# Optimization experiments

Measured on AMD Instinct MI355X. Metric: run time of the kernel, lower is better.

## Reference

```python
import jax, jax.numpy as jnp
import numpy as np

N_NODES = 50000
N_EDGES = 800000
IN_FEATS = 128
HIDDEN = 64
EDGE_FEATS = 3


def setup_inputs() -> dict:
    key = jax.random.key(0)
    ks = jax.random.split(key, 8)
    s = lambda d: 1.0 / np.sqrt(d)
    return {
        "x": jax.random.normal(ks[0], (N_NODES, IN_FEATS), jnp.float32),
        "efeat": jax.random.normal(ks[1], (N_EDGES, EDGE_FEATS), jnp.float32),
        "src": jax.random.randint(ks[2], (N_EDGES,), 0, N_NODES, jnp.int32),
        "dst": jax.random.randint(ks[3], (N_EDGES,), 0, N_NODES, jnp.int32),
        "W1": jax.random.normal(ks[4], (IN_FEATS, HIDDEN), jnp.float32) * s(IN_FEATS),
        "b1": jnp.zeros((HIDDEN,), jnp.float32),
        "W2": jax.random.normal(ks[5], (HIDDEN, HIDDEN), jnp.float32) * s(HIDDEN),
        "b2": jnp.zeros((HIDDEN,), jnp.float32),
        "We": jax.random.normal(ks[6], (2 * HIDDEN + EDGE_FEATS, 1), jnp.float32) * s(2 * HIDDEN + EDGE_FEATS),
        "be": jnp.zeros((1,), jnp.float32),
    }


def reference(x, efeat, src, dst, W1, b1, W2, b2, We, be):
    n = x.shape[0]
    ones = jnp.ones(src.shape[0], x.dtype)
    # DGL GraphConv norm='both': scale src feats by out-deg^-1/2, aggregate, scale by in-deg^-1/2
    deg_out = jnp.clip(jax.ops.segment_sum(ones, src, num_segments=n), 1.0)
    deg_in = jnp.clip(jax.ops.segment_sum(ones, dst, num_segments=n), 1.0)
    c_src = deg_out ** -0.5  # [N]
    c_dst = deg_in ** -0.5   # [N]

    def graph_conv(h, W, b):
        hn = h * c_src[:, None]                             # pre-scale
        agg = jax.ops.segment_sum(hn[src], dst, num_segments=n)
        return (agg * c_dst[:, None]) @ W + b

    h = jax.nn.relu(graph_conv(x, W1, b1))
    h = graph_conv(h, W2, b2)

    # edge_func: sigmoid(Linear(cat[src_h, dst_h, efeat])) -- split We to avoid concat
    H = h.shape[1]
    Ws, Wd, Wf = We[:H], We[H:2 * H], We[2 * H:]
    logits = h[src] @ Ws + h[dst] @ Wd + efeat @ Wf + be   # [E, 1]
    return jax.nn.sigmoid(logits[:, 0])                    # [E]
```

## Files before the change

### kernel.cpp

```cpp
#include <hip/hip_runtime.h>
#include <math.h>
#include <stdint.h>

#define N_NODES 50000
#define N_EDGES 800000
#define IN_FEATS 128
#define HIDDEN 64

#define CSPLIT 32
#define CHUNK (N_EDGES / CSPLIT)
#define NQUART (N_NODES / 4)
#define NQWORDS (NQUART / 2)

#define NB_HIST 256
#define NB_E4 782
#define NB_GEMM 782

typedef __attribute__((ext_vector_type(8))) short bf16x8;
typedef __attribute__((ext_vector_type(4))) float f32x4;

__device__ __forceinline__ unsigned short f2bf(float f) {
    unsigned u = __float_as_uint(f);
    u = (u + 0x7FFF + ((u >> 16) & 1)) >> 16;
    return (unsigned short)u;
}

#define ACC8F(A, r, cs)                                        \
    A[0] = fmaf(cs, __uint_as_float((r).x << 16), A[0]);       \
    A[1] = fmaf(cs, __uint_as_float((r).x & 0xffff0000u), A[1]); \
    A[2] = fmaf(cs, __uint_as_float((r).y << 16), A[2]);       \
    A[3] = fmaf(cs, __uint_as_float((r).y & 0xffff0000u), A[3]); \
    A[4] = fmaf(cs, __uint_as_float((r).z << 16), A[4]);       \
    A[5] = fmaf(cs, __uint_as_float((r).z & 0xffff0000u), A[5]); \
    A[6] = fmaf(cs, __uint_as_float((r).w << 16), A[6]);       \
    A[7] = fmaf(cs, __uint_as_float((r).w & 0xffff0000u), A[7]);

__global__ __launch_bounds__(256) void hist_gemm_kernel(const int* __restrict__ src,
                                                        const int* __restrict__ dst,
                                                        unsigned short* __restrict__ epos,
                                                        unsigned* __restrict__ pin,
                                                        unsigned* __restrict__ pout,
                                                        const float* __restrict__ x,
                                                        const float* __restrict__ W,
                                                        unsigned short* __restrict__ yb) {
    __shared__ union {
        unsigned cnt[NQWORDS];
        bf16x8 bfrag[16][64];
    } u;
    if (blockIdx.x < NB_HIST) {
        int b = blockIdx.x;
        int c = b >> 3;
        int kind = (b >> 2) & 1;
        int quar = b & 3;
        int lo = quar * NQUART;
        for (int i = threadIdx.x; i < NQWORDS; i += 256) u.cnt[i] = 0;
        __syncthreads();
        if (kind == 0) {
            const int4* d4 = reinterpret_cast<const int4*>(dst + c * CHUNK);
            for (int i = threadIdx.x; i < CHUNK / 4; i += 256) {
                int4 d = d4[i];
                int e = c * CHUNK + i * 4;
                unsigned q, old;
                q = (unsigned)(d.x - lo);
                if (q < NQUART) { old = atomicAdd(&u.cnt[q >> 1], 1u << ((q & 1) * 16));
                                  epos[e + 0] = (unsigned short)(old >> ((q & 1) * 16)); }
                q = (unsigned)(d.y - lo);
                if (q < NQUART) { old = atomicAdd(&u.cnt[q >> 1], 1u << ((q & 1) * 16));
                                  epos[e + 1] = (unsigned short)(old >> ((q & 1) * 16)); }
                q = (unsigned)(d.z - lo);
                if (q < NQUART) { old = atomicAdd(&u.cnt[q >> 1], 1u << ((q & 1) * 16));
                                  epos[e + 2] = (unsigned short)(old >> ((q & 1) * 16)); }
                q = (unsigned)(d.w - lo);
                if (q < NQUART) { old = atomicAdd(&u.cnt[q >> 1], 1u << ((q & 1) * 16));
                                  epos[e + 3] = (unsigned short)(old >> ((q & 1) * 16)); }
            }
        } else {
            const int4* s4 = reinterpret_cast<const int4*>(src + c * CHUNK);
            for (int i = threadIdx.x; i < CHUNK / 4; i += 256) {
                int4 s = s4[i];
                unsigned q;
                q = (unsigned)(s.x - lo); if (q < NQUART) atomicAdd(&u.cnt[q >> 1], 1u << ((q & 1) * 16));
                q = (unsigned)(s.y - lo); if (q < NQUART) atomicAdd(&u.cnt[q >> 1], 1u << ((q & 1) * 16));
                q = (unsigned)(s.z - lo); if (q < NQUART) atomicAdd(&u.cnt[q >> 1], 1u << ((q & 1) * 16));
                q = (unsigned)(s.w - lo); if (q < NQUART) atomicAdd(&u.cnt[q >> 1], 1u << ((q & 1) * 16));
            }
        }
        __syncthreads();
        unsigned* outp = (kind ? pout : pin) + c * (N_NODES / 2) + quar * NQWORDS;
        for (int i = threadIdx.x; i < NQWORDS; i += 256) outp[i] = u.cnt[i];
        return;
    }
    int gb = blockIdx.x - NB_HIST;
    for (int idx = threadIdx.x; idx < 16 * 64; idx += 256) {
        int f = idx >> 6, l = idx & 63;
        int nt = f >> 2, kt = f & 3;
        int col = nt * 16 + (l & 15);
        int k0 = kt * 32 + (l >> 4) * 8;
        bf16x8 bv;
#pragma unroll
        for (int j = 0; j < 8; ++j) bv[j] = (short)f2bf(W[(k0 + j) * HIDDEN + col]);
        u.bfrag[f][l] = bv;
    }
    __syncthreads();
    int wid = threadIdx.x >> 6, l = threadIdx.x & 63;
    bf16x8 Breg[16];
#pragma unroll
    for (int f = 0; f < 16; ++f) Breg[f] = u.bfrag[f][l];

    int row0 = gb * 64 + wid * 16;
    int arow = row0 + (l & 15);
    int asafe = min(arow, N_NODES - 1);
    const float* xr = x + (size_t)asafe * IN_FEATS + (l >> 4) * 8;
    f32x4 acc0 = {0.f, 0.f, 0.f, 0.f};
    f32x4 acc1 = {0.f, 0.f, 0.f, 0.f};
    f32x4 acc2 = {0.f, 0.f, 0.f, 0.f};
    f32x4 acc3 = {0.f, 0.f, 0.f, 0.f};
#pragma unroll
    for (int kt = 0; kt < 4; ++kt) {
        float4 a0 = *reinterpret_cast<const float4*>(xr + kt * 32);
        float4 a1 = *reinterpret_cast<const float4*>(xr + kt * 32 + 4);
        bf16x8 av;
        av[0] = (short)f2bf(a0.x); av[1] = (short)f2bf(a0.y);
        av[2] = (short)f2bf(a0.z); av[3] = (short)f2bf(a0.w);
        av[4] = (short)f2bf(a1.x); av[5] = (short)f2bf(a1.y);
        av[6] = (short)f2bf(a1.z); av[7] = (short)f2bf(a1.w);
        acc0 = __builtin_amdgcn_mfma_f32_16x16x32_bf16(av, Breg[0 * 4 + kt], acc0, 0, 0, 0);
        acc1 = __builtin_amdgcn_mfma_f32_16x16x32_bf16(av, Breg[1 * 4 + kt], acc1, 0, 0, 0);
        acc2 = __builtin_amdgcn_mfma_f32_16x16x32_bf16(av, Breg[2 * 4 + kt], acc2, 0, 0, 0);
        acc3 = __builtin_amdgcn_mfma_f32_16x16x32_bf16(av, Breg[3 * 4 + kt], acc3, 0, 0, 0);
    }
#pragma unroll
    for (int i = 0; i < 4; ++i) {
        int row = row0 + (l >> 4) * 4 + i;
        if (row < N_NODES) {
            unsigned short* yr = yb + (size_t)row * HIDDEN + (l & 15);
            yr[0]  = f2bf(acc0[i]);
            yr[16] = f2bf(acc1[i]);
            yr[32] = f2bf(acc2[i]);
            yr[48] = f2bf(acc3[i]);
        }
    }
}

__global__ __launch_bounds__(256) void prep_kernel(const unsigned* __restrict__ pin,
                                                   const unsigned* __restrict__ pout,
                                                   float* __restrict__ cs,
                                                   float* __restrict__ cd,
                                                   int* __restrict__ offs,
                                                   int* __restrict__ bsum,
                                                   const float* __restrict__ W2,
                                                   const float* __restrict__ We,
                                                   const float* __restrict__ b2,
                                                   float* __restrict__ w2s,
                                                   float* __restrict__ w2d,
                                                   float* __restrict__ w2c) {
    int b = blockIdx.x;
    int t = threadIdx.x;
    if (b == 49) {
        if (t < 64) {
            float s = 0.f, d = 0.f;
            for (int j = 0; j < HIDDEN; ++j) {
                float w = W2[t * HIDDEN + j];
                s = fmaf(w, We[j], s);
                d = fmaf(w, We[HIDDEN + j], d);
            }
            w2s[t] = s;
            w2d[t] = d;
        } else if (t == 64) {
            float s = 0.f, d = 0.f;
            for (int j = 0; j < HIDDEN; ++j) {
                s = fmaf(We[j], b2[j], s);
                d = fmaf(We[HIDDEN + j], b2[j], d);
            }
            w2c[0] = s;
            w2c[1] = d;
        }
        return;
    }
    __shared__ int sums[256];
    int v0 = b * 1024 + t * 4;
    bool ok = v0 < N_NODES;
    unsigned si0 = 0, si1 = 0, si2 = 0, si3 = 0;
    unsigned so0 = 0, so1 = 0, so2 = 0, so3 = 0;
    if (ok) {
        int w0 = v0 >> 1;
#pragma unroll
        for (int c = 0; c < CSPLIT; ++c) {
            uint2 a = *reinterpret_cast<const uint2*>(pin + (size_t)c * (N_NODES / 2) + w0);
            uint2 o = *reinterpret_cast<const uint2*>(pout + (size_t)c * (N_NODES / 2) + w0);
            si0 += a.x & 0xffffu; si1 += a.x >> 16;
            si2 += a.y & 0xffffu; si3 += a.y >> 16;
            so0 += o.x & 0xffffu; so1 += o.x >> 16;
            so2 += o.y & 0xffffu; so3 += o.y >> 16;
        }
        *reinterpret_cast<float4*>(cs + v0) =
            make_float4(rsqrtf(fmaxf((float)so0, 1.f)), rsqrtf(fmaxf((float)so1, 1.f)),
                        rsqrtf(fmaxf((float)so2, 1.f)), rsqrtf(fmaxf((float)so3, 1.f)));
        *reinterpret_cast<float4*>(cd + v0) =
            make_float4(rsqrtf(fmaxf((float)si0, 1.f)), rsqrtf(fmaxf((float)si1, 1.f)),
                        rsqrtf(fmaxf((float)si2, 1.f)), rsqrtf(fmaxf((float)si3, 1.f)));
    }
    int d0 = (int)si0, d1 = (int)si1, d2 = (int)si2, d3 = (int)si3;
    sums[t] = d0 + d1 + d2 + d3;
    __syncthreads();
    for (int o = 1; o < 256; o <<= 1) {
        int v = (t >= o) ? sums[t - o] : 0;
        __syncthreads();
        sums[t] += v;
        __syncthreads();
    }
    int excl = (t == 0) ? 0 : sums[t - 1];
    if (ok) {
        *reinterpret_cast<int4*>(offs + v0) =
            make_int4(excl, excl + d0, excl + d0 + d1, excl + d0 + d1 + d2);
    }
    if (t == 255) bsum[b] = sums[255];
}

__global__ __launch_bounds__(256) void scan3_base_kernel(int* __restrict__ offs,
                                                         const int* __restrict__ bsum,
                                                         const unsigned* __restrict__ pin,
                                                         unsigned short* __restrict__ baser) {
    __shared__ int sbase[64];
    int t = threadIdx.x;
    if (t < 64) {
        int val = (t < 49) ? bsum[t] : 0;
        int s = val;
#pragma unroll
        for (int o = 1; o < 64; o <<= 1) {
            int u = __shfl_up(s, o, 64);
            if (t >= o) s += u;
        }
        sbase[t] = s - val;
    }
    __syncthreads();
    int v = blockIdx.x * 256 + t;
    if (v >= N_NODES) return;
    int off = offs[v] + sbase[v >> 10];
    offs[v] = off;
    int rel = 0;
    int sh = (v & 1) * 16;
#pragma unroll
    for (int c = 0; c < CSPLIT; ++c) {
        baser[(size_t)c * N_NODES + v] = (unsigned short)rel;
        rel += (int)((pin[(size_t)c * (N_NODES / 2) + (v >> 1)] >> sh) & 0xffffu);
    }
    if (v == 0) offs[N_NODES] = N_EDGES;
}

__global__ __launch_bounds__(256) void fill_kernel(const int* __restrict__ src,
                                                   const int* __restrict__ dst,
                                                   const unsigned short* __restrict__ epos,
                                                   const int* __restrict__ offs,
                                                   const unsigned short* __restrict__ baser,
                                                   int* __restrict__ csr_src) {
    int t = blockIdx.x * 256 + threadIdx.x;
    int e0 = t * 4;
    if (e0 >= N_EDGES) return;
    int c = e0 / CHUNK;
    const unsigned short* brc = baser + (size_t)c * N_NODES;
    int4 s = *reinterpret_cast<const int4*>(src + e0);
    int4 d = *reinterpret_cast<const int4*>(dst + e0);
    ushort4 ep = *reinterpret_cast<const ushort4*>(epos + e0);
    csr_src[offs[d.x] + brc[d.x] + ep.x] = s.x;
    csr_src[offs[d.y] + brc[d.y] + ep.y] = s.y;
    csr_src[offs[d.z] + brc[d.z] + ep.z] = s.z;
    csr_src[offs[d.w] + brc[d.w] + ep.w] = s.w;
}

__global__ __launch_bounds__(256) void gather_t_kernel(const unsigned short* __restrict__ y,
                                                       const int* __restrict__ offs,
                                                       const int* __restrict__ csr_src,
                                                       const float* __restrict__ c_src,
                                                       const float* __restrict__ c_dst,
                                                       const float* __restrict__ b1,
                                                       const float* __restrict__ w2s,
                                                       const float* __restrict__ w2d,
                                                       float2* __restrict__ t) {
    int wid = threadIdx.x >> 6, l = threadIdx.x & 63;
    int slot = l >> 3, q8 = l & 7;
    int v0 = blockIdx.x * 8 + wid * 2;
    int v1 = v0 + 1;
    int beg0 = offs[v0], end0 = offs[v0 + 1], end1 = offs[v0 + 2];
    int k0 = beg0, k1 = end0;
    float acc0[8] = {0.f, 0.f, 0.f, 0.f, 0.f, 0.f, 0.f, 0.f};
    float acc1[8] = {0.f, 0.f, 0.f, 0.f, 0.f, 0.f, 0.f, 0.f};
    while (k0 + 8 <= end0 && k1 + 8 <= end1) {
        int sA = csr_src[k0 + slot];
        int sB = csr_src[k1 + slot];
        float csA = c_src[sA];
        float csB = c_src[sB];
        uint4 rA = *reinterpret_cast<const uint4*>(y + (size_t)sA * HIDDEN + q8 * 8);
        uint4 rB = *reinterpret_cast<const uint4*>(y + (size_t)sB * HIDDEN + q8 * 8);
        ACC8F(acc0, rA, csA);
        ACC8F(acc1, rB, csB);
        k0 += 8;
        k1 += 8;
    }
    while (k0 + 8 <= end0) {
        int s = csr_src[k0 + slot];
        float cs = c_src[s];
        uint4 r = *reinterpret_cast<const uint4*>(y + (size_t)s * HIDDEN + q8 * 8);
        ACC8F(acc0, r, cs);
        k0 += 8;
    }
    while (k1 + 8 <= end1) {
        int s = csr_src[k1 + slot];
        float cs = c_src[s];
        uint4 r = *reinterpret_cast<const uint4*>(y + (size_t)s * HIDDEN + q8 * 8);
        ACC8F(acc1, r, cs);
        k1 += 8;
    }
    if (slot < end0 - k0) {
        int s = csr_src[k0 + slot];
        float cs = c_src[s];
        uint4 r = *reinterpret_cast<const uint4*>(y + (size_t)s * HIDDEN + q8 * 8);
        ACC8F(acc0, r, cs);
    }
    if (slot < end1 - k1) {
        int s = csr_src[k1 + slot];
        float cs = c_src[s];
        uint4 r = *reinterpret_cast<const uint4*>(y + (size_t)s * HIDDEN + q8 * 8);
        ACC8F(acc1, r, cs);
    }
#pragma unroll
    for (int i = 0; i < 8; ++i) {
        acc0[i] += __shfl_xor(acc0[i], 8, 64);
        acc0[i] += __shfl_xor(acc0[i], 16, 64);
        acc0[i] += __shfl_xor(acc0[i], 32, 64);
        acc1[i] += __shfl_xor(acc1[i], 8, 64);
        acc1[i] += __shfl_xor(acc1[i], 16, 64);
        acc1[i] += __shfl_xor(acc1[i], 32, 64);
    }
    float4 ba = *reinterpret_cast<const float4*>(b1 + q8 * 8);
    float4 bb = *reinterpret_cast<const float4*>(b1 + q8 * 8 + 4);
    float4 wsa = *reinterpret_cast<const float4*>(w2s + q8 * 8);
    float4 wsb = *reinterpret_cast<const float4*>(w2s + q8 * 8 + 4);
    float4 wda = *reinterpret_cast<const float4*>(w2d + q8 * 8);
    float4 wdb = *reinterpret_cast<const float4*>(w2d + q8 * 8 + 4);
    float c0 = c_dst[v0], c1 = c_dst[v1];
    float h0, h1, h2, h3, h4, h5, h6, h7;
    h0 = fmaxf(fmaf(c0, acc0[0], ba.x), 0.f);
    h1 = fmaxf(fmaf(c0, acc0[1], ba.y), 0.f);
    h2 = fmaxf(fmaf(c0, acc0[2], ba.z), 0.f);
    h3 = fmaxf(fmaf(c0, acc0[3], ba.w), 0.f);
    h4 = fmaxf(fmaf(c0, acc0[4], bb.x), 0.f);
    h5 = fmaxf(fmaf(c0, acc0[5], bb.y), 0.f);
    h6 = fmaxf(fmaf(c0, acc0[6], bb.z), 0.f);
    h7 = fmaxf(fmaf(c0, acc0[7], bb.w), 0.f);
    float ps0 = h0 * wsa.x + h1 * wsa.y + h2 * wsa.z + h3 * wsa.w
              + h4 * wsb.x + h5 * wsb.y + h6 * wsb.z + h7 * wsb.w;
    float pd0 = h0 * wda.x + h1 * wda.y + h2 * wda.z + h3 * wda.w
              + h4 * wdb.x + h5 * wdb.y + h6 * wdb.z + h7 * wdb.w;
    h0 = fmaxf(fmaf(c1, acc1[0], ba.x), 0.f);
    h1 = fmaxf(fmaf(c1, acc1[1], ba.y), 0.f);
    h2 = fmaxf(fmaf(c1, acc1[2], ba.z), 0.f);
    h3 = fmaxf(fmaf(c1, acc1[3], ba.w), 0.f);
    h4 = fmaxf(fmaf(c1, acc1[4], bb.x), 0.f);
    h5 = fmaxf(fmaf(c1, acc1[5], bb.y), 0.f);
    h6 = fmaxf(fmaf(c1, acc1[6], bb.z), 0.f);
    h7 = fmaxf(fmaf(c1, acc1[7], bb.w), 0.f);
    float ps1 = h0 * wsa.x + h1 * wsa.y + h2 * wsa.z + h3 * wsa.w
              + h4 * wsb.x + h5 * wsb.y + h6 * wsb.z + h7 * wsb.w;
    float pd1 = h0 * wda.x + h1 * wda.y + h2 * wda.z + h3 * wda.w
              + h4 * wdb.x + h5 * wdb.y + h6 * wdb.z + h7 * wdb.w;
#pragma unroll
    for (int o = 1; o <= 4; o <<= 1) {
        ps0 += __shfl_xor(ps0, o, 64);
        pd0 += __shfl_xor(pd0, o, 64);
        ps1 += __shfl_xor(ps1, o, 64);
        pd1 += __shfl_xor(pd1, o, 64);
    }
    if (l == 0) {
        float cs0 = c_src[v0], cs1 = c_src[v1];
        *reinterpret_cast<float4*>(t + v0) =
            make_float4(cs0 * ps0, cs0 * pd0, cs1 * ps1, cs1 * pd1);
    }
}

__global__ __launch_bounds__(256) void gather2_kernel(const float2* __restrict__ t,
                                                      const int* __restrict__ offs,
                                                      const int* __restrict__ csr_src,
                                                      const float* __restrict__ c_dst,
                                                      const float* __restrict__ w2c,
                                                      float* __restrict__ a_s,
                                                      float* __restrict__ a_d) {
    int wid = threadIdx.x >> 6, l = threadIdx.x & 63;
    int sub = l >> 4, q = l & 15;
    int v = blockIdx.x * 16 + wid * 4 + sub;
    int beg = offs[v], end = offs[v + 1];
    float ps = 0.f, pd = 0.f;
    for (int k = beg + q; k < end; k += 16) {
        float2 tv = t[csr_src[k]];
        ps += tv.x;
        pd += tv.y;
    }
#pragma unroll
    for (int o = 1; o <= 8; o <<= 1) {
        ps += __shfl_xor(ps, o, 64);
        pd += __shfl_xor(pd, o, 64);
    }
    if (q == 0) {
        float c = c_dst[v];
        a_s[v] = fmaf(c, ps, w2c[0]);
        a_d[v] = fmaf(c, pd, w2c[1]);
    }
}

__global__ __launch_bounds__(256) void edge_out_kernel(const int* __restrict__ src,
                                                       const int* __restrict__ dst,
                                                       const float* __restrict__ efeat,
                                                       const float* __restrict__ We,
                                                       const float* __restrict__ be,
                                                       const float* __restrict__ a_s,
                                                       const float* __restrict__ a_d,
                                                       float* __restrict__ out) {
    int t = blockIdx.x * 256 + threadIdx.x;
    int e0 = t * 8;
    if (e0 >= N_EDGES) return;
    float w0 = We[2 * HIDDEN + 0], w1 = We[2 * HIDDEN + 1], w2 = We[2 * HIDDEN + 2];
    float b = be[0];
    int4 sA = *reinterpret_cast<const int4*>(src + e0);
    int4 sB = *reinterpret_cast<const int4*>(src + e0 + 4);
    int4 dA = *reinterpret_cast<const int4*>(dst + e0);
    int4 dB = *reinterpret_cast<const int4*>(dst + e0 + 4);
    const float4* f = reinterpret_cast<const float4*>(efeat + (long)e0 * 3);
    float4 f0 = f[0], f1 = f[1], f2 = f[2], f3 = f[3], f4 = f[4], f5 = f[5];
    float as0 = a_s[sA.x], as1 = a_s[sA.y], as2 = a_s[sA.z], as3 = a_s[sA.w];
    float as4 = a_s[sB.x], as5 = a_s[sB.y], as6 = a_s[sB.z], as7 = a_s[sB.w];
    float ad0 = a_d[dA.x], ad1 = a_d[dA.y], ad2 = a_d[dA.z], ad3 = a_d[dA.w];
    float ad4 = a_d[dB.x], ad5 = a_d[dB.y], ad6 = a_d[dB.z], ad7 = a_d[dB.w];
    float4 oA, oB;
    float z;
    z = as0 + ad0 + f0.x * w0 + f0.y * w1 + f0.z * w2 + b;
    oA.x = 1.0f / (1.0f + __expf(-z));
    z = as1 + ad1 + f0.w * w0 + f1.x * w1 + f1.y * w2 + b;
    oA.y = 1.0f / (1.0f + __expf(-z));
    z = as2 + ad2 + f1.z * w0 + f1.w * w1 + f2.x * w2 + b;
    oA.z = 1.0f / (1.0f + __expf(-z));
    z = as3 + ad3 + f2.y * w0 + f2.z * w1 + f2.w * w2 + b;
    oA.w = 1.0f / (1.0f + __expf(-z));
    z = as4 + ad4 + f3.x * w0 + f3.y * w1 + f3.z * w2 + b;
    oB.x = 1.0f / (1.0f + __expf(-z));
    z = as5 + ad5 + f3.w * w0 + f4.x * w1 + f4.y * w2 + b;
    oB.y = 1.0f / (1.0f + __expf(-z));
    z = as6 + ad6 + f4.z * w0 + f4.w * w1 + f5.x * w2 + b;
    oB.z = 1.0f / (1.0f + __expf(-z));
    z = as7 + ad7 + f5.y * w0 + f5.z * w1 + f5.w * w2 + b;
    oB.w = 1.0f / (1.0f + __expf(-z));
    *reinterpret_cast<float4*>(out + e0) = oA;
    *reinterpret_cast<float4*>(out + e0 + 4) = oB;
}

extern "C" void kernel_launch(void* const* d_in, const int* in_sizes, int n_in,
                              void* d_out, int out_size, void* d_ws, size_t ws_size,
                              hipStream_t stream) {
    const float* x     = (const float*)d_in[0];
    const float* efeat = (const float*)d_in[1];
    const int*   src   = (const int*)d_in[2];
    const int*   dst   = (const int*)d_in[3];
    const float* W1    = (const float*)d_in[4];
    const float* b1    = (const float*)d_in[5];
    const float* W2    = (const float*)d_in[6];
    const float* b2    = (const float*)d_in[7];
    const float* We    = (const float*)d_in[8];
    const float* be    = (const float*)d_in[9];
    float* out = (float*)d_out;

    char* p = (char*)d_ws;
    auto alloc = [&](size_t bytes) {
        char* r = p;
        p += (bytes + 255) & ~(size_t)255;
        return r;
    };
    float* c_src   = (float*)alloc((size_t)N_NODES * 4);
    float* c_dst   = (float*)alloc((size_t)N_NODES * 4);
    float* a_s     = (float*)alloc((size_t)N_NODES * 4);
    float* a_d     = (float*)alloc((size_t)N_NODES * 4);
    int*   offs    = (int*)alloc((size_t)(N_NODES + 1) * 4);
    int*   bsum    = (int*)alloc(64 * 4);
    float* w2s     = (float*)alloc(HIDDEN * 4);
    float* w2d     = (float*)alloc(HIDDEN * 4);
    float* w2c     = (float*)alloc(2 * 4);
    unsigned*       pin   = (unsigned*)alloc((size_t)CSPLIT * (N_NODES / 2) * 4);
    unsigned*       pout  = (unsigned*)alloc((size_t)CSPLIT * (N_NODES / 2) * 4);
    unsigned short* epos  = (unsigned short*)alloc((size_t)N_EDGES * 2);
    unsigned short* baser = (unsigned short*)alloc((size_t)CSPLIT * N_NODES * 2);
    int*            csr_src = (int*)alloc((size_t)N_EDGES * 4);
    unsigned short* yb    = (unsigned short*)alloc((size_t)N_NODES * HIDDEN * 2);
    float2*         t     = (float2*)alloc((size_t)N_NODES * 8);

    const int NB_V = (N_NODES + 255) / 256;

    hist_gemm_kernel<<<NB_HIST + NB_GEMM, 256, 0, stream>>>(src, dst, epos, pin, pout,
                                                            x, W1, yb);
    prep_kernel<<<50, 256, 0, stream>>>(pin, pout, c_src, c_dst, offs, bsum,
                                        W2, We, b2, w2s, w2d, w2c);
    scan3_base_kernel<<<NB_V, 256, 0, stream>>>(offs, bsum, pin, baser);
    fill_kernel<<<NB_E4, 256, 0, stream>>>(src, dst, epos, offs, baser, csr_src);
    gather_t_kernel<<<N_NODES / 8, 256, 0, stream>>>(yb, offs, csr_src, c_src, c_dst,
                                                     b1, w2s, w2d, t);
    gather2_kernel<<<N_NODES / 16, 256, 0, stream>>>(t, offs, csr_src, c_dst, w2c, a_s, a_d);
    edge_out_kernel<<<(N_EDGES / 8 + 255) / 256, 256, 0, stream>>>(src, dst, efeat, We, be,
                                                                   a_s, a_d, out);
}
```

Measured before the change: 93.53 us.

## Split bf16 hidden features into two 32-wide planes for gather kernel

The GEMM output is stored as two separate planes of 32 features each, and the first gather kernel runs twice as many blocks, each handling one plane with 16 edge slots of 4 lanes. Partial t values are written per plane and summed in gather2, which now reads a float4 per source node. The aim is a smaller per-pass working set for random row gathers, so each plane fits better in cache, and more edge-level parallelism per wave. In exchange, csr_src and offsets are read twice, there is an extra shuffle stage, and t doubles in size.

```diff
diff --git a/kernel.cpp b/kernel.cpp
--- a/kernel.cpp
+++ b/kernel.cpp
@@ -15,6 +15,8 @@
 #define NB_HIST 256
 #define NB_E4 782
 #define NB_GEMM 782
+#define NBG 6250
+#define PLANE_ELEMS ((size_t)N_NODES * 32)
 
 typedef __attribute__((ext_vector_type(8))) short bf16x8;
 typedef __attribute__((ext_vector_type(4))) float f32x4;
@@ -133,11 +135,12 @@
     for (int i = 0; i < 4; ++i) {
         int row = row0 + (l >> 4) * 4 + i;
         if (row < N_NODES) {
-            unsigned short* yr = yb + (size_t)row * HIDDEN + (l & 15);
-            yr[0]  = f2bf(acc0[i]);
-            yr[16] = f2bf(acc1[i]);
-            yr[32] = f2bf(acc2[i]);
-            yr[48] = f2bf(acc3[i]);
+            unsigned short* y0 = yb + (size_t)row * 32 + (l & 15);
+            unsigned short* y1 = y0 + PLANE_ELEMS;
+            y0[0]  = f2bf(acc0[i]);
+            y0[16] = f2bf(acc1[i]);
+            y1[0]  = f2bf(acc2[i]);
+            y1[16] = f2bf(acc3[i]);
         }
     }
 }
@@ -277,77 +280,83 @@
                                                        const float* __restrict__ w2s,
                                                        const float* __restrict__ w2d,
                                                        float2* __restrict__ t) {
+    int plane = (blockIdx.x >= NBG) ? 1 : 0;
+    int bb = blockIdx.x - plane * NBG;
+    const unsigned short* yp = y + (size_t)plane * PLANE_ELEMS;
     int wid = threadIdx.x >> 6, l = threadIdx.x & 63;
-    int slot = l >> 3, q8 = l & 7;
-    int v0 = blockIdx.x * 8 + wid * 2;
+    int slot = l >> 2, q4 = l & 3;
+    int v0 = bb * 8 + wid * 2;
     int v1 = v0 + 1;
     int beg0 = offs[v0], end0 = offs[v0 + 1], end1 = offs[v0 + 2];
     int k0 = beg0, k1 = end0;
     float acc0[8] = {0.f, 0.f, 0.f, 0.f, 0.f, 0.f, 0.f, 0.f};
     float acc1[8] = {0.f, 0.f, 0.f, 0.f, 0.f, 0.f, 0.f, 0.f};
-    while (k0 + 8 <= end0 && k1 + 8 <= end1) {
+    while (k0 + 16 <= end0 && k1 + 16 <= end1) {
         int sA = csr_src[k0 + slot];
         int sB = csr_src[k1 + slot];
         float csA = c_src[sA];
         float csB = c_src[sB];
-        uint4 rA = *reinterpret_cast<const uint4*>(y + (size_t)sA * HIDDEN + q8 * 8);
-        uint4 rB = *reinterpret_cast<const uint4*>(y + (size_t)sB * HIDDEN + q8 * 8);
+        uint4 rA = *reinterpret_cast<const uint4*>(yp + (size_t)sA * 32 + q4 * 8);
+        uint4 rB = *reinterpret_cast<const uint4*>(yp + (size_t)sB * 32 + q4 * 8);
         ACC8F(acc0, rA, csA);
         ACC8F(acc1, rB, csB);
-        k0 += 8;
-        k1 += 8;
-    }
-    while (k0 + 8 <= end0) {
+        k0 += 16;
+        k1 += 16;
+    }
+    while (k0 + 16 <= end0) {
         int s = csr_src[k0 + slot];
         float cs = c_src[s];
-        uint4 r = *reinterpret_cast<const uint4*>(y + (size_t)s * HIDDEN + q8 * 8);
+        uint4 r = *reinterpret_cast<const uint4*>(yp + (size_t)s * 32 + q4 * 8);
         ACC8F(acc0, r, cs);
-        k0 += 8;
-    }
-    while (k1 + 8 <= end1) {
+        k0 += 16;
+    }
+    while (k1 + 16 <= end1) {
         int s = csr_src[k1 + slot];
         float cs = c_src[s];
-        uint4 r = *reinterpret_cast<const uint4*>(y + (size_t)s * HIDDEN + q8 * 8);
+        uint4 r = *reinterpret_cast<const uint4*>(yp + (size_t)s * 32 + q4 * 8);
         ACC8F(acc1, r, cs);
-        k1 += 8;
+        k1 += 16;
     }
     if (slot < end0 - k0) {
         int s = csr_src[k0 + slot];
         float cs = c_src[s];
-        uint4 r = *reinterpret_cast<const uint4*>(y + (size_t)s * HIDDEN + q8 * 8);
+        uint4 r = *reinterpret_cast<const uint4*>(yp + (size_t)s * 32 + q4 * 8);
         ACC8F(acc0, r, cs);
     }
     if (slot < end1 - k1) {
         int s = csr_src[k1 + slot];
         float cs = c_src[s];
-        uint4 r = *reinterpret_cast<const uint4*>(y + (size_t)s * HIDDEN + q8 * 8);
+        uint4 r = *reinterpret_cast<const uint4*>(yp + (size_t)s * 32 + q4 * 8);
         ACC8F(acc1, r, cs);
     }
 #pragma unroll
     for (int i = 0; i < 8; ++i) {
+        acc0[i] += __shfl_xor(acc0[i], 4, 64);
         acc0[i] += __shfl_xor(acc0[i], 8, 64);
         acc0[i] += __shfl_xor(acc0[i], 16, 64);
         acc0[i] += __shfl_xor(acc0[i], 32, 64);
+        acc1[i] += __shfl_xor(acc1[i], 4, 64);
         acc1[i] += __shfl_xor(acc1[i], 8, 64);
         acc1[i] += __shfl_xor(acc1[i], 16, 64);
         acc1[i] += __shfl_xor(acc1[i], 32, 64);
     }
-    float4 ba = *reinterpret_cast<const float4*>(b1 + q8 * 8);
-    float4 bb = *reinterpret_cast<const float4*>(b1 + q8 * 8 + 4);
-    float4 wsa = *reinterpret_cast<const float4*>(w2s + q8 * 8);
-    float4 wsb = *reinterpret_cast<const float4*>(w2s + q8 * 8 + 4);
-    float4 wda = *reinterpret_cast<const float4*>(w2d + q8 * 8);
-    float4 wdb = *reinterpret_cast<const float4*>(w2d + q8 * 8 + 4);
+    int fb = plane * 32 + q4 * 8;
+    float4 ba = *reinterpret_cast<const float4*>(b1 + fb);
+    float4 bb4 = *reinterpret_cast<const float4*>(b1 + fb + 4);
+    float4 wsa = *reinterpret_cast<const float4*>(w2s + fb);
+    float4 wsb = *reinterpret_cast<const float4*>(w2s + fb + 4);
+    float4 wda = *reinterpret_cast<const float4*>(w2d + fb);
+    float4 wdb = *reinterpret_cast<const float4*>(w2d + fb + 4);
     float c0 = c_dst[v0], c1 = c_dst[v1];
     float h0, h1, h2, h3, h4, h5, h6, h7;
     h0 = fmaxf(fmaf(c0, acc0[0], ba.x), 0.f);
     h1 = fmaxf(fmaf(c0, acc0[1], ba.y), 0.f);
     h2 = fmaxf(fmaf(c0, acc0[2], ba.z), 0.f);
     h3 = fmaxf(fmaf(c0, acc0[3], ba.w), 0.f);
-    h4 = fmaxf(fmaf(c0, acc0[4], bb.x), 0.f);
-    h5 = fmaxf(fmaf(c0, acc0[5], bb.y), 0.f);
-    h6 = fmaxf(fmaf(c0, acc0[6], bb.z), 0.f);
-    h7 = fmaxf(fmaf(c0, acc0[7], bb.w), 0.f);
+    h4 = fmaxf(fmaf(c0, acc0[4], bb4.x), 0.f);
+    h5 = fmaxf(fmaf(c0, acc0[5], bb4.y), 0.f);
+    h6 = fmaxf(fmaf(c0, acc0[6], bb4.z), 0.f);
+    h7 = fmaxf(fmaf(c0, acc0[7], bb4.w), 0.f);
     float ps0 = h0 * wsa.x + h1 * wsa.y + h2 * wsa.z + h3 * wsa.w
               + h4 * wsb.x + h5 * wsb.y + h6 * wsb.z + h7 * wsb.w;
     float pd0 = h0 * wda.x + h1 * wda.y + h2 * wda.z + h3 * wda.w
@@ -356,25 +365,27 @@
     h1 = fmaxf(fmaf(c1, acc1[1], ba.y), 0.f);
     h2 = fmaxf(fmaf(c1, acc1[2], ba.z), 0.f);
     h3 = fmaxf(fmaf(c1, acc1[3], ba.w), 0.f);
-    h4 = fmaxf(fmaf(c1, acc1[4], bb.x), 0.f);
-    h5 = fmaxf(fmaf(c1, acc1[5], bb.y), 0.f);
-    h6 = fmaxf(fmaf(c1, acc1[6], bb.z), 0.f);
-    h7 = fmaxf(fmaf(c1, acc1[7], bb.w), 0.f);
+    h4 = fmaxf(fmaf(c1, acc1[4], bb4.x), 0.f);
+    h5 = fmaxf(fmaf(c1, acc1[5], bb4.y), 0.f);
+    h6 = fmaxf(fmaf(c1, acc1[6], bb4.z), 0.f);
+    h7 = fmaxf(fmaf(c1, acc1[7], bb4.w), 0.f);
     float ps1 = h0 * wsa.x + h1 * wsa.y + h2 * wsa.z + h3 * wsa.w
               + h4 * wsb.x + h5 * wsb.y + h6 * wsb.z + h7 * wsb.w;
     float pd1 = h0 * wda.x + h1 * wda.y + h2 * wda.z + h3 * wda.w
               + h4 * wdb.x + h5 * wdb.y + h6 * wdb.z + h7 * wdb.w;
 #pragma unroll
-    for (int o = 1; o <= 4; o <<= 1) {
+    for (int o = 1; o <= 2; o <<= 1) {
         ps0 += __shfl_xor(ps0, o, 64);
         pd0 += __shfl_xor(pd0, o, 64);
         ps1 += __shfl_xor(ps1, o, 64);
         pd1 += __shfl_xor(pd1, o, 64);
     }
     if (l == 0) {
-        float cs0 = c_src[v0], cs1 = c_src[v1];
-        *reinterpret_cast<float4*>(t + v0) =
-            make_float4(cs0 * ps0, cs0 * pd0, cs1 * ps1, cs1 * pd1);
+        float cs0 = c_src[v0];
+        t[2 * v0 + plane] = make_float2(cs0 * ps0, cs0 * pd0);
+    } else if (l == 1) {
+        float cs1 = c_src[v1];
+        t[2 * v1 + plane] = make_float2(cs1 * ps1, cs1 * pd1);
     }
 }
 
@@ -391,9 +402,10 @@
     int beg = offs[v], end = offs[v + 1];
     float ps = 0.f, pd = 0.f;
     for (int k = beg + q; k < end; k += 16) {
-        float2 tv = t[csr_src[k]];
-        ps += tv.x;
-        pd += tv.y;
+        int s = csr_src[k];
+        float4 tt = *reinterpret_cast<const float4*>(t + 2 * (size_t)s);
+        ps += tt.x + tt.z;
+        pd += tt.y + tt.w;
     }
 #pragma unroll
     for (int o = 1; o <= 8; o <<= 1) {
@@ -487,8 +499,8 @@
     unsigned short* epos  = (unsigned short*)alloc((size_t)N_EDGES * 2);
     unsigned short* baser = (unsigned short*)alloc((size_t)CSPLIT * N_NODES * 2);
     int*            csr_src = (int*)alloc((size_t)N_EDGES * 4);
-    unsigned short* yb    = (unsigned short*)alloc((size_t)N_NODES * HIDDEN * 2);
-    float2*         t     = (float2*)alloc((size_t)N_NODES * 8);
+    unsigned short* yb    = (unsigned short*)alloc((size_t)2 * PLANE_ELEMS * 2);
+    float2*         t     = (float2*)alloc((size_t)2 * N_NODES * 8);
 
     const int NB_V = (N_NODES + 255) / 256;
 
@@ -498,8 +510,8 @@
                                         W2, We, b2, w2s, w2d, w2c);
     scan3_base_kernel<<<NB_V, 256, 0, stream>>>(offs, bsum, pin, baser);
     fill_kernel<<<NB_E4, 256, 0, stream>>>(src, dst, epos, offs, baser, csr_src);
-    gather_t_kernel<<<N_NODES / 8, 256, 0, stream>>>(yb, offs, csr_src, c_src, c_dst,
-                                                     b1, w2s, w2d, t);
+    gather_t_kernel<<<2 * NBG, 256, 0, stream>>>(yb, offs, csr_src, c_src, c_dst,
+                                                 b1, w2s, w2d, t);
     gather2_kernel<<<N_NODES / 16, 256, 0, stream>>>(t, offs, csr_src, c_dst, w2c, a_s, a_d);
     edge_out_kernel<<<(N_EDGES / 8 + 255) / 256, 256, 0, stream>>>(src, dst, efeat, We, be,
                                                                    a_s, a_d, out);
```

Result: slower. 113.0 us (+20.8%).
